# Kernel optimization log

Hardware: AMD Instinct MI355X
Metric: run time of the kernel (lower is better)

The kernel has to match this reference:

```python
import jax, jax.numpy as jnp
import numpy as np

EMBED = 1024
HEADS = 16
HEAD_DIM = EMBED // HEADS
EPS = 1e-8


def setup_inputs() -> dict:
    key = jax.random.key(0)
    ks = jax.random.split(key, 10)
    s = 1.0 / np.sqrt(EMBED)
    return {
        "hidden_input": jax.random.normal(ks[0], (4, 2048, EMBED), dtype=jnp.float32),
        "Wq": jax.random.uniform(ks[1], (EMBED, EMBED), jnp.float32, -s, s),
        "bq": jax.random.uniform(ks[2], (EMBED,), jnp.float32, -s, s),
        "Wk": jax.random.uniform(ks[3], (EMBED, EMBED), jnp.float32, -s, s),
        "bk": jax.random.uniform(ks[4], (EMBED,), jnp.float32, -s, s),
        "Wv": jax.random.uniform(ks[5], (EMBED, EMBED), jnp.float32, -s, s),
        "bv": jax.random.uniform(ks[6], (EMBED,), jnp.float32, -s, s),
        "Wp": jax.random.uniform(ks[7], (EMBED, EMBED), jnp.float32, -s, s),
        "bp": jax.random.uniform(ks[8], (EMBED,), jnp.float32, -s, s),
        "gamma": jnp.ones((EMBED,), jnp.float32),
        "beta": jnp.zeros((EMBED,), jnp.float32),
    }


def reference(hidden_input, Wq, bq, Wk, bk, Wv, bv, Wp, bp, gamma, beta):
    n, l, e = hidden_input.shape
    h, d = HEADS, HEAD_DIM

    def split_heads(x):  # [n, l, e] -> [n, h, l, d]
        return x.reshape(n, l, h, d).transpose(0, 2, 1, 3)

    q = split_heads(hidden_input @ Wq + bq)
    k = split_heads(hidden_input @ Wk + bk)
    v = split_heads(hidden_input @ Wv + bv)

    scores = jnp.einsum("nhqd,nhkd->nhqk", q, k) / jnp.sqrt(jnp.float32(d))
    attn = jax.nn.softmax(scores, axis=-1)
    ctx = jnp.einsum("nhqk,nhkd->nhqd", attn, v)
    ctx = ctx.transpose(0, 2, 1, 3).reshape(n, l, e)

    out = ctx @ Wp + bp
    x = out + hidden_input
    mu = jnp.mean(x, axis=-1, keepdims=True)
    var = jnp.mean(jnp.square(x - mu), axis=-1, keepdims=True)
    return (x - mu) / jnp.sqrt(var + EPS) * gamma + beta
```

## Files before the change

### kernel.cpp

```cpp
#include <hip/hip_runtime.h>

#define EMBED 1024
#define SEQ   2048
#define BATCH 4
#define HEADS 16

typedef __attribute__((ext_vector_type(8))) short short8;
typedef __attribute__((ext_vector_type(4))) float floatx4;
typedef __attribute__((ext_vector_type(16))) float floatx16;

#define MFMA16(a, b, c) __builtin_amdgcn_mfma_f32_16x16x32_bf16((a), (b), (c), 0, 0, 0)
#define MFMA32(a, b, c) __builtin_amdgcn_mfma_f32_32x32x16_bf16((a), (b), (c), 0, 0, 0)
#define ATT_SCALE (0.125f * 1.44269504088896340736f)

static __device__ __forceinline__ unsigned short f2bf(float f) {
  union { float f; unsigned int u; } v; v.f = f;
  unsigned int u = v.u;
  u += 0x7fffu + ((u >> 16) & 1u);
  return (unsigned short)(u >> 16);
}

static __device__ __forceinline__ unsigned cvtpk(float lo, float hi) {
  unsigned r;
  asm("v_cvt_pk_bf16_f32 %0, %1, %2" : "=v"(r) : "v"(lo), "v"(hi));
  return r;
}

static __device__ __forceinline__ void async16(const unsigned short* g, unsigned short* l) {
  __builtin_amdgcn_global_load_lds(
      (const __attribute__((address_space(1))) void*)g,
      (__attribute__((address_space(3))) void*)l, 16, 0, 0);
}

__global__ __launch_bounds__(256) void k_prep(const float* __restrict__ hid,
                                              unsigned short* __restrict__ hidA,
                                              const float* __restrict__ Wq, const float* __restrict__ Wk,
                                              const float* __restrict__ Wv, const float* __restrict__ Wp,
                                              unsigned short* __restrict__ WT) {
  __shared__ unsigned short tile[64][65];
  const int bid = blockIdx.x, tid = threadIdx.x;
  if (bid < 4096) {
    int i = bid * 256 + tid;
    const float4* s = (const float4*)hid;
    float4 a = s[i * 2], b = s[i * 2 + 1];
    uint4 o;
    o.x = (unsigned)f2bf(a.x) | ((unsigned)f2bf(a.y) << 16);
    o.y = (unsigned)f2bf(a.z) | ((unsigned)f2bf(a.w) << 16);
    o.z = (unsigned)f2bf(b.x) | ((unsigned)f2bf(b.y) << 16);
    o.w = (unsigned)f2bf(b.z) | ((unsigned)f2bf(b.w) << 16);
    ((uint4*)hidA)[i] = o;
    return;
  }
  const int idx = bid - 4096;
  const int z = idx >> 8, rem = idx & 255;
  const float* src = (z == 0) ? Wq : (z == 1) ? Wk : (z == 2) ? Wv : Wp;
  unsigned short* dst = WT + (size_t)z * EMBED * EMBED;
  const int k0 = (rem & 15) * 64, n0 = (rem >> 4) * 64;
  for (int i = tid; i < 4096; i += 256) {
    int r = i >> 6, c = i & 63;
    tile[c][r] = f2bf(src[(size_t)(k0 + r) * EMBED + n0 + c]);
  }
  __syncthreads();
  for (int i = tid; i < 4096; i += 256) {
    int r = i >> 6, c = i & 63;
    dst[(size_t)(n0 + r) * EMBED + k0 + c] = tile[r][c];
  }
}

__global__ __launch_bounds__(256) void k_gemm_qkv(const unsigned short* __restrict__ A,
                                                  const unsigned short* __restrict__ BT,
                                                  const float* __restrict__ bq,
                                                  const float* __restrict__ bk,
                                                  const float* __restrict__ bv,
                                                  unsigned short* __restrict__ C) {
  __shared__ unsigned short Als[128 * 64];
  __shared__ unsigned short Bls[128 * 64];
  const int tid = threadIdx.x;
  const int m0 = blockIdx.x * 128, n0 = blockIdx.y * 128;
  const int w = tid >> 6, lane = tid & 63, l16 = lane & 15, quad = lane >> 4;
  const int l7 = l16 & 7;
  const int wrow = (w >> 1) * 64, wcol = (w & 1) * 64;

  floatx4 acc[4][4];
#pragma unroll
  for (int i = 0; i < 4; ++i)
#pragma unroll
    for (int j = 0; j < 4; ++j) acc[i][j] = {0.f, 0.f, 0.f, 0.f};

  const int srow = tid >> 3;
  const int scol = (((tid & 7) ^ (srow & 7)) * 8);
  const unsigned short* Ap = A + (size_t)(m0 + srow) * EMBED + scol;
  const unsigned short* Bp = BT + (size_t)(n0 + srow) * EMBED + scol;

  int ab[2], bb[2];
#pragma unroll
  for (int kc = 0; kc < 2; ++kc) {
    ab[kc] = (wrow + l16) * 64 + (((4 * kc + quad) ^ l7) << 3);
    bb[kc] = (wcol + l16) * 64 + (((4 * kc + quad) ^ l7) << 3);
  }

  for (int kt = 0; kt < 16; ++kt) {
    const int k0 = kt * 64;
#pragma unroll
    for (int i = 0; i < 4; ++i)
      async16(Ap + k0 + (size_t)i * 32 * EMBED, Als + i * 2048 + tid * 8);
#pragma unroll
    for (int i = 0; i < 4; ++i)
      async16(Bp + k0 + (size_t)i * 32 * EMBED, Bls + i * 2048 + tid * 8);
    __syncthreads();
    short8 af[4][2], bf[4][2];
#pragma unroll
    for (int mt = 0; mt < 4; ++mt)
#pragma unroll
      for (int kc = 0; kc < 2; ++kc)
        af[mt][kc] = *(const short8*)(Als + ab[kc] + mt * 1024);
#pragma unroll
    for (int nt = 0; nt < 4; ++nt)
#pragma unroll
      for (int kc = 0; kc < 2; ++kc)
        bf[nt][kc] = *(const short8*)(Bls + bb[kc] + nt * 1024);
#pragma unroll
    for (int kc = 0; kc < 2; ++kc)
#pragma unroll
      for (int mt = 0; mt < 4; ++mt)
#pragma unroll
        for (int nt = 0; nt < 4; ++nt)
          acc[mt][nt] = MFMA16(af[mt][kc], bf[nt][kc], acc[mt][nt]);
    __syncthreads();
  }

  const float* bsel = (n0 < 1024) ? bq : (n0 < 2048 ? bk : bv);
  const float scl = (n0 < 1024) ? ATT_SCALE : 1.0f;
  const int nb = n0 & 1023;
  float bias[4];
#pragma unroll
  for (int nt = 0; nt < 4; ++nt) bias[nt] = bsel[nb + wcol + nt * 16 + l16];
#pragma unroll
  for (int mt = 0; mt < 4; ++mt)
#pragma unroll
    for (int r = 0; r < 4; ++r) {
      int gm = m0 + wrow + mt * 16 + quad * 4 + r;
      size_t base = (size_t)gm * 3072 + n0 + wcol;
#pragma unroll
      for (int nt = 0; nt < 4; ++nt)
        C[base + nt * 16 + l16] = f2bf((acc[mt][nt][r] + bias[nt]) * scl);
    }
}

__global__ __launch_bounds__(256) void k_vt(const unsigned short* __restrict__ QKV,
                                            unsigned short* __restrict__ VT) {
  int lt = blockIdx.x;
  int bh = blockIdx.y;
  int b = bh >> 4, h = bh & 15;
  int l0 = lt * 64;
  __shared__ unsigned short tile[64][65];
  const unsigned short* src = QKV + (size_t)(b * SEQ) * 3072 + 2048 + h * 64;
  unsigned short* dst = VT + (size_t)bh * 64 * SEQ;
  int tid = threadIdx.x;
  for (int i = tid; i < 4096; i += 256) {
    int r = i >> 6, c = i & 63;
    tile[c][r] = src[(size_t)(l0 + r) * 3072 + c];
  }
  __syncthreads();
  for (int i = tid; i < 4096; i += 256) {
    int r = i >> 6, c = i & 63;
    dst[(size_t)r * SEQ + l0 + c] = tile[r][c];
  }
}

__global__ __launch_bounds__(256, 2) void k_attn(const unsigned short* __restrict__ QKV,
                                                 const unsigned short* __restrict__ VT,
                                                 unsigned short* __restrict__ CTX) {
  const int bh = blockIdx.x, qt = blockIdx.y;
  const int b = bh >> 4, h = bh & 15;
  const int tid = threadIdx.x;
  const int w = tid >> 6, lane = tid & 63;
  const int l32 = lane & 31, hi = lane >> 5;

  __shared__ unsigned short Kls[2][64 * 64];
  __shared__ unsigned short Vls[2][64 * 64];
  __shared__ float rsls[4][64];

  const unsigned short* Qb = QKV + (size_t)(b * SEQ + qt * 256 + w * 64) * 3072 + h * 64;
  const unsigned short* Kb = QKV + (size_t)(b * SEQ) * 3072 + 1024 + h * 64;
  const unsigned short* Vb = VT + (size_t)bh * 64 * SEQ;

  short8 qf[2][4];
#pragma unroll
  for (int qg = 0; qg < 2; ++qg)
#pragma unroll
    for (int ds = 0; ds < 4; ++ds)
      qf[qg][ds] = *(const short8*)(Qb + (size_t)(qg * 32 + l32) * 3072 + ds * 16 + hi * 8);

  floatx16 o[2][2];
  float rs[2] = {0.f, 0.f};
#pragma unroll
  for (int qg = 0; qg < 2; ++qg)
#pragma unroll
    for (int dg = 0; dg < 2; ++dg)
#pragma unroll
      for (int c = 0; c < 16; ++c) o[qg][dg][c] = 0.f;

  const int srow = tid >> 3;
  const int scol = (((tid & 7) ^ (srow & 7)) * 8);

  async16(Kb + (size_t)srow * 3072 + scol, Kls[0] + tid * 8);
  async16(Kb + (size_t)(32 + srow) * 3072 + scol, Kls[0] + 2048 + tid * 8);
  async16(Vb + (size_t)srow * SEQ + scol, Vls[0] + tid * 8);
  async16(Vb + (size_t)(32 + srow) * SEQ + scol, Vls[0] + 2048 + tid * 8);
  __syncthreads();

  int cur = 0;
  for (int kt = 0; kt < 32; ++kt) {
    if (kt < 31) {
      const int kn = (kt + 1) * 64;
      unsigned short* Kd = Kls[cur ^ 1];
      unsigned short* Vd = Vls[cur ^ 1];
      async16(Kb + (size_t)(kn + srow) * 3072 + scol, Kd + tid * 8);
      async16(Kb + (size_t)(kn + 32 + srow) * 3072 + scol, Kd + 2048 + tid * 8);
      async16(Vb + (size_t)srow * SEQ + kn + scol, Vd + tid * 8);
      async16(Vb + (size_t)(32 + srow) * SEQ + kn + scol, Vd + 2048 + tid * 8);
    }
    const unsigned short* Kc = Kls[cur];
    const unsigned short* Vc = Vls[cur];

    short8 pa[2][4];
#pragma unroll
    for (int kvg = 0; kvg < 2; ++kvg) {
      short8 kf[4];
#pragma unroll
      for (int ds = 0; ds < 4; ++ds) {
        const int row = kvg * 32 + l32;
        kf[ds] = *(const short8*)(Kc + row * 64 + (((ds * 2 + hi) ^ (row & 7)) << 3));
      }
#pragma unroll
      for (int qg = 0; qg < 2; ++qg) {
        floatx16 s;
#pragma unroll
        for (int c = 0; c < 16; ++c) s[c] = 0.f;
#pragma unroll
        for (int ds = 0; ds < 4; ++ds) s = MFMA32(kf[ds], qf[qg][ds], s);
        float p[16];
#pragma unroll
        for (int c = 0; c < 16; ++c) p[c] = __builtin_amdgcn_exp2f(s[c]);
        rs[qg] += (((p[0] + p[1]) + (p[2] + p[3])) + ((p[4] + p[5]) + (p[6] + p[7])))
                + (((p[8] + p[9]) + (p[10] + p[11])) + ((p[12] + p[13]) + (p[14] + p[15])));
#pragma unroll
        for (int half = 0; half < 2; ++half) {
          unsigned w0 = cvtpk(p[half * 8 + 0], p[half * 8 + 1]);
          unsigned w1 = cvtpk(p[half * 8 + 2], p[half * 8 + 3]);
          unsigned w2 = cvtpk(p[half * 8 + 4], p[half * 8 + 5]);
          unsigned w3 = cvtpk(p[half * 8 + 6], p[half * 8 + 7]);
          asm("v_permlane32_swap_b32 %0, %1" : "+v"(w0), "+v"(w2));
          asm("v_permlane32_swap_b32 %0, %1" : "+v"(w1), "+v"(w3));
          union { unsigned u[4]; short8 s8; } pk;
          pk.u[0] = w0; pk.u[1] = w1; pk.u[2] = w2; pk.u[3] = w3;
          pa[qg][kvg * 2 + half] = pk.s8;
        }
      }
    }

#pragma unroll
    for (int dg = 0; dg < 2; ++dg) {
      short8 vf[4];
#pragma unroll
      for (int ks = 0; ks < 4; ++ks) {
        const int row = dg * 32 + l32;
        vf[ks] = *(const short8*)(Vc + row * 64 + (((ks * 2 + hi) ^ (row & 7)) << 3));
      }
#pragma unroll
      for (int qg = 0; qg < 2; ++qg)
#pragma unroll
        for (int ks = 0; ks < 4; ++ks)
          o[qg][dg] = MFMA32(pa[qg][ks], vf[ks], o[qg][dg]);
    }

    __syncthreads();
    cur ^= 1;
  }

  rs[0] += __shfl_xor(rs[0], 32);
  rs[1] += __shfl_xor(rs[1], 32);
  if (lane < 32) {
    rsls[w][l32] = rs[0];
    rsls[w][32 + l32] = rs[1];
  }

#pragma unroll
  for (int qg = 0; qg < 2; ++qg)
#pragma unroll
    for (int j = 0; j < 16; ++j) {
      const int rl = (j & 3) + 8 * (j >> 2) + 4 * hi;
      const float inv = 1.f / rsls[w][qg * 32 + rl];
      const int gq = b * SEQ + qt * 256 + w * 64 + qg * 32 + rl;
      const size_t base = (size_t)gq * EMBED + h * 64;
#pragma unroll
      for (int dg = 0; dg < 2; ++dg)
        CTX[base + dg * 32 + l32] = f2bf(o[qg][dg][j] * inv);
    }
}

__global__ __launch_bounds__(256) void k_gemm_proj(const unsigned short* __restrict__ A,
                                                   const unsigned short* __restrict__ BT,
                                                   const float* __restrict__ bp,
                                                   const float* __restrict__ hid,
                                                   float* __restrict__ X) {
  __shared__ unsigned short Als[128 * 64];
  __shared__ unsigned short Bls[128 * 64];
  const int tid = threadIdx.x;
  const int m0 = blockIdx.x * 128, n0 = blockIdx.y * 128;
  const int w = tid >> 6, lane = tid & 63, l16 = lane & 15, quad = lane >> 4;
  const int l7 = l16 & 7;
  const int wrow = (w >> 1) * 64, wcol = (w & 1) * 64;

  floatx4 acc[4][4];
#pragma unroll
  for (int i = 0; i < 4; ++i)
#pragma unroll
    for (int j = 0; j < 4; ++j) acc[i][j] = {0.f, 0.f, 0.f, 0.f};

  const int srow = tid >> 3;
  const int scol = (((tid & 7) ^ (srow & 7)) * 8);
  const unsigned short* Ap = A + (size_t)(m0 + srow) * EMBED + scol;
  const unsigned short* Bp = BT + (size_t)(n0 + srow) * EMBED + scol;

  int ab[2], bb[2];
#pragma unroll
  for (int kc = 0; kc < 2; ++kc) {
    ab[kc] = (wrow + l16) * 64 + (((4 * kc + quad) ^ l7) << 3);
    bb[kc] = (wcol + l16) * 64 + (((4 * kc + quad) ^ l7) << 3);
  }

  for (int kt = 0; kt < 16; ++kt) {
    const int k0 = kt * 64;
#pragma unroll
    for (int i = 0; i < 4; ++i)
      async16(Ap + k0 + (size_t)i * 32 * EMBED, Als + i * 2048 + tid * 8);
#pragma unroll
    for (int i = 0; i < 4; ++i)
      async16(Bp + k0 + (size_t)i * 32 * EMBED, Bls + i * 2048 + tid * 8);
    __syncthreads();
    short8 af[4][2], bf[4][2];
#pragma unroll
    for (int mt = 0; mt < 4; ++mt)
#pragma unroll
      for (int kc = 0; kc < 2; ++kc)
        af[mt][kc] = *(const short8*)(Als + ab[kc] + mt * 1024);
#pragma unroll
    for (int nt = 0; nt < 4; ++nt)
#pragma unroll
      for (int kc = 0; kc < 2; ++kc)
        bf[nt][kc] = *(const short8*)(Bls + bb[kc] + nt * 1024);
#pragma unroll
    for (int kc = 0; kc < 2; ++kc)
#pragma unroll
      for (int mt = 0; mt < 4; ++mt)
#pragma unroll
        for (int nt = 0; nt < 4; ++nt)
          acc[mt][nt] = MFMA16(af[mt][kc], bf[nt][kc], acc[mt][nt]);
    __syncthreads();
  }

  float bias[4];
#pragma unroll
  for (int nt = 0; nt < 4; ++nt) bias[nt] = bp[n0 + wcol + nt * 16 + l16];
#pragma unroll
  for (int mt = 0; mt < 4; ++mt)
#pragma unroll
    for (int r = 0; r < 4; ++r) {
      int gm = m0 + wrow + mt * 16 + quad * 4 + r;
      size_t base = (size_t)gm * EMBED + n0 + wcol;
#pragma unroll
      for (int nt = 0; nt < 4; ++nt) {
        size_t idx = base + nt * 16 + l16;
        X[idx] = acc[mt][nt][r] + bias[nt] + hid[idx];
      }
    }
}

__global__ __launch_bounds__(256) void k_ln(float* __restrict__ x,
                                            const float* __restrict__ gamma,
                                            const float* __restrict__ beta) {
  int row = blockIdx.x, tid = threadIdx.x;
  float4* rp = (float4*)(x + (size_t)row * EMBED);
  float4 v = rp[tid];
  float s = v.x + v.y + v.z + v.w;
  float q = v.x * v.x + v.y * v.y + v.z * v.z + v.w * v.w;
#pragma unroll
  for (int off = 1; off < 64; off <<= 1) {
    s += __shfl_xor(s, off);
    q += __shfl_xor(q, off);
  }
  __shared__ float ss[4], sq[4];
  int w = tid >> 6;
  if ((tid & 63) == 0) { ss[w] = s; sq[w] = q; }
  __syncthreads();
  s = ss[0] + ss[1] + ss[2] + ss[3];
  q = sq[0] + sq[1] + sq[2] + sq[3];
  float mean = s * (1.f / 1024.f);
  float var = q * (1.f / 1024.f) - mean * mean;
  float rstd = rsqrtf(var + 1e-8f);
  float4 g = ((const float4*)gamma)[tid];
  float4 be = ((const float4*)beta)[tid];
  v.x = (v.x - mean) * rstd * g.x + be.x;
  v.y = (v.y - mean) * rstd * g.y + be.y;
  v.z = (v.z - mean) * rstd * g.z + be.z;
  v.w = (v.w - mean) * rstd * g.w + be.w;
  rp[tid] = v;
}

extern "C" void kernel_launch(void* const* d_in, const int* in_sizes, int n_in,
                              void* d_out, int out_size, void* d_ws, size_t ws_size,
                              hipStream_t stream) {
  const float* hid   = (const float*)d_in[0];
  const float* Wq    = (const float*)d_in[1];
  const float* bq    = (const float*)d_in[2];
  const float* Wk    = (const float*)d_in[3];
  const float* bk    = (const float*)d_in[4];
  const float* Wv    = (const float*)d_in[5];
  const float* bv    = (const float*)d_in[6];
  const float* Wp    = (const float*)d_in[7];
  const float* bp    = (const float*)d_in[8];
  const float* gamma = (const float*)d_in[9];
  const float* beta  = (const float*)d_in[10];
  float* out = (float*)d_out;

  char* ws = (char*)d_ws;
  unsigned short* hidA = (unsigned short*)ws;
  unsigned short* WT   = (unsigned short*)(ws + (size_t)(16 << 20));
  unsigned short* QKV  = (unsigned short*)(ws + (size_t)(24 << 20));
  unsigned short* VT   = (unsigned short*)(ws + (size_t)(72 << 20));
  unsigned short* CTX  = (unsigned short*)(ws + (size_t)(88 << 20));

  k_prep<<<5120, 256, 0, stream>>>(hid, hidA, Wq, Wk, Wv, Wp, WT);
  k_gemm_qkv<<<dim3(64, 24), 256, 0, stream>>>(hidA, WT, bq, bk, bv, QKV);
  k_vt<<<dim3(32, 64), 256, 0, stream>>>(QKV, VT);
  k_attn<<<dim3(64, 8), 256, 0, stream>>>(QKV, VT, CTX);
  k_gemm_proj<<<dim3(64, 8), 256, 0, stream>>>(CTX, WT + (size_t)3 * EMBED * EMBED, bp, hid, out);
  k_ln<<<8192, 256, 0, stream>>>(out, gamma, beta);
}
```

Before: 279.3 us.

## Split attention KV range across two blocks and add a combine kernel

The attention kernel now splits the 2048-key range into two halves along a new grid z dimension. Each half writes an unnormalized bf16 partial context and its per-row exp sums to workspace. A new k_comb kernel adds the two partials, normalizes them and writes CTX. Launch bounds rise to 4 blocks per CU to double parallelism and occupancy. The cost is extra global traffic and a launch for the partials, a bf16 rounding step on unnormalized partials, and possible register pressure or spills from the tighter launch bound.

```diff
diff --git a/kernel.cpp b/kernel.cpp
--- a/kernel.cpp
+++ b/kernel.cpp
@@ -18,6 +18,13 @@
   unsigned int u = v.u;
   u += 0x7fffu + ((u >> 16) & 1u);
   return (unsigned short)(u >> 16);
+}
+
+static __device__ __forceinline__ float bf2f_lo(unsigned u) {
+  union { unsigned u; float f; } v; v.u = u << 16; return v.f;
+}
+static __device__ __forceinline__ float bf2f_hi(unsigned u) {
+  union { unsigned u; float f; } v; v.u = u & 0xffff0000u; return v.f;
 }
 
 static __device__ __forceinline__ unsigned cvtpk(float lo, float hi) {
@@ -168,10 +175,12 @@
   }
 }
 
-__global__ __launch_bounds__(256, 2) void k_attn(const unsigned short* __restrict__ QKV,
+__global__ __launch_bounds__(256, 4) void k_attn(const unsigned short* __restrict__ QKV,
                                                  const unsigned short* __restrict__ VT,
-                                                 unsigned short* __restrict__ CTX) {
-  const int bh = blockIdx.x, qt = blockIdx.y;
+                                                 unsigned short* __restrict__ OP0,
+                                                 unsigned short* __restrict__ OP1,
+                                                 float* __restrict__ RSP) {
+  const int bh = blockIdx.x, qt = blockIdx.y, hv = blockIdx.z;
   const int b = bh >> 4, h = bh & 15;
   const int tid = threadIdx.x;
   const int w = tid >> 6, lane = tid & 63;
@@ -179,7 +188,6 @@
 
   __shared__ unsigned short Kls[2][64 * 64];
   __shared__ unsigned short Vls[2][64 * 64];
-  __shared__ float rsls[4][64];
 
   const unsigned short* Qb = QKV + (size_t)(b * SEQ + qt * 256 + w * 64) * 3072 + h * 64;
   const unsigned short* Kb = QKV + (size_t)(b * SEQ) * 3072 + 1024 + h * 64;
@@ -203,17 +211,21 @@
 
   const int srow = tid >> 3;
   const int scol = (((tid & 7) ^ (srow & 7)) * 8);
-
-  async16(Kb + (size_t)srow * 3072 + scol, Kls[0] + tid * 8);
-  async16(Kb + (size_t)(32 + srow) * 3072 + scol, Kls[0] + 2048 + tid * 8);
-  async16(Vb + (size_t)srow * SEQ + scol, Vls[0] + tid * 8);
-  async16(Vb + (size_t)(32 + srow) * SEQ + scol, Vls[0] + 2048 + tid * 8);
+  const int kbase = hv * 16;
+
+  {
+    const int kv0 = kbase * 64;
+    async16(Kb + (size_t)(kv0 + srow) * 3072 + scol, Kls[0] + tid * 8);
+    async16(Kb + (size_t)(kv0 + 32 + srow) * 3072 + scol, Kls[0] + 2048 + tid * 8);
+    async16(Vb + (size_t)srow * SEQ + kv0 + scol, Vls[0] + tid * 8);
+    async16(Vb + (size_t)(32 + srow) * SEQ + kv0 + scol, Vls[0] + 2048 + tid * 8);
+  }
   __syncthreads();
 
   int cur = 0;
-  for (int kt = 0; kt < 32; ++kt) {
-    if (kt < 31) {
-      const int kn = (kt + 1) * 64;
+  for (int kt = 0; kt < 16; ++kt) {
+    if (kt < 15) {
+      const int kn = (kbase + kt + 1) * 64;
       unsigned short* Kd = Kls[cur ^ 1];
       unsigned short* Vd = Vls[cur ^ 1];
       async16(Kb + (size_t)(kn + srow) * 3072 + scol, Kd + tid * 8);
@@ -282,22 +294,45 @@
   rs[0] += __shfl_xor(rs[0], 32);
   rs[1] += __shfl_xor(rs[1], 32);
   if (lane < 32) {
-    rsls[w][l32] = rs[0];
-    rsls[w][32 + l32] = rs[1];
-  }
-
+    float* rp = RSP + ((size_t)(hv * 64 + bh)) * SEQ + qt * 256 + w * 64;
+    rp[l32] = rs[0];
+    rp[32 + l32] = rs[1];
+  }
+
+  unsigned short* Od = hv ? OP1 : OP0;
 #pragma unroll
   for (int qg = 0; qg < 2; ++qg)
 #pragma unroll
     for (int j = 0; j < 16; ++j) {
       const int rl = (j & 3) + 8 * (j >> 2) + 4 * hi;
-      const float inv = 1.f / rsls[w][qg * 32 + rl];
       const int gq = b * SEQ + qt * 256 + w * 64 + qg * 32 + rl;
       const size_t base = (size_t)gq * EMBED + h * 64;
 #pragma unroll
       for (int dg = 0; dg < 2; ++dg)
-        CTX[base + dg * 32 + l32] = f2bf(o[qg][dg][j] * inv);
-    }
+        Od[base + dg * 32 + l32] = f2bf(o[qg][dg][j]);
+    }
+}
+
+__global__ __launch_bounds__(256) void k_comb(const unsigned short* __restrict__ OP0,
+                                              const unsigned short* __restrict__ OP1,
+                                              const float* __restrict__ RSP,
+                                              unsigned short* __restrict__ CTX) {
+  const int gq = blockIdx.x, tid = threadIdx.x;
+  const int b = gq >> 11, q = gq & 2047;
+  const int col = tid * 4, h = col >> 6;
+  const float inv = 1.f / (RSP[((size_t)(b * 16 + h)) * SEQ + q] +
+                           RSP[((size_t)(64 + b * 16 + h)) * SEQ + q]);
+  const size_t base = (size_t)gq * EMBED + col;
+  uint2 ua = *(const uint2*)(OP0 + base);
+  uint2 ub = *(const uint2*)(OP1 + base);
+  float c0 = (bf2f_lo(ua.x) + bf2f_lo(ub.x)) * inv;
+  float c1 = (bf2f_hi(ua.x) + bf2f_hi(ub.x)) * inv;
+  float c2 = (bf2f_lo(ua.y) + bf2f_lo(ub.y)) * inv;
+  float c3 = (bf2f_hi(ua.y) + bf2f_hi(ub.y)) * inv;
+  uint2 oo;
+  oo.x = (unsigned)f2bf(c0) | ((unsigned)f2bf(c1) << 16);
+  oo.y = (unsigned)f2bf(c2) | ((unsigned)f2bf(c3) << 16);
+  *(uint2*)(CTX + base) = oo;
 }
 
 __global__ __launch_bounds__(256) void k_gemm_proj(const unsigned short* __restrict__ A,
@@ -431,11 +466,15 @@
   unsigned short* QKV  = (unsigned short*)(ws + (size_t)(24 << 20));
   unsigned short* VT   = (unsigned short*)(ws + (size_t)(72 << 20));
   unsigned short* CTX  = (unsigned short*)(ws + (size_t)(88 << 20));
+  unsigned short* OP0  = (unsigned short*)ws;
+  unsigned short* OP1  = (unsigned short*)(ws + (size_t)(104 << 20));
+  float*          RSP  = (float*)(ws + (size_t)(120 << 20));
 
   k_prep<<<5120, 256, 0, stream>>>(hid, hidA, Wq, Wk, Wv, Wp, WT);
   k_gemm_qkv<<<dim3(64, 24), 256, 0, stream>>>(hidA, WT, bq, bk, bv, QKV);
   k_vt<<<dim3(32, 64), 256, 0, stream>>>(QKV, VT);
-  k_attn<<<dim3(64, 8), 256, 0, stream>>>(QKV, VT, CTX);
+  k_attn<<<dim3(64, 8, 2), 256, 0, stream>>>(QKV, VT, OP0, OP1, RSP);
+  k_comb<<<8192, 256, 0, stream>>>(OP0, OP1, RSP, CTX);
   k_gemm_proj<<<dim3(64, 8), 256, 0, stream>>>(CTX, WT + (size_t)3 * EMBED * EMBED, bp, hid, out);
   k_ln<<<8192, 256, 0, stream>>>(out, gamma, beta);
 }
```

Measured after the change: 748.6 us. 2.68x slower.

## Halve attention query tile per block to 128 rows, doubling grid and occupancy

Applied to the files above, without the earlier changes.

Each wave in the attention kernel now handles 32 query rows instead of 64, so a block covers 128 queries and the grid doubles to 1024 blocks. Launch bounds rise to 3 blocks per CU because each wave holds fewer accumulators and Q fragments. The aim is more parallelism and occupancy on the 256-CU device, since the previous 512-block grid underfilled it. The cost is that each K/V tile loaded into LDS is reused by half as many queries, which doubles total K/V traffic.

```diff
diff --git a/kernel.cpp b/kernel.cpp
--- a/kernel.cpp
+++ b/kernel.cpp
@@ -168,7 +168,7 @@
   }
 }
 
-__global__ __launch_bounds__(256, 2) void k_attn(const unsigned short* __restrict__ QKV,
+__global__ __launch_bounds__(256, 3) void k_attn(const unsigned short* __restrict__ QKV,
                                                  const unsigned short* __restrict__ VT,
                                                  unsigned short* __restrict__ CTX) {
   const int bh = blockIdx.x, qt = blockIdx.y;
@@ -179,27 +179,23 @@
 
   __shared__ unsigned short Kls[2][64 * 64];
   __shared__ unsigned short Vls[2][64 * 64];
-  __shared__ float rsls[4][64];
-
-  const unsigned short* Qb = QKV + (size_t)(b * SEQ + qt * 256 + w * 64) * 3072 + h * 64;
+  __shared__ float rsls[4][32];
+
+  const unsigned short* Qb = QKV + (size_t)(b * SEQ + qt * 128 + w * 32) * 3072 + h * 64;
   const unsigned short* Kb = QKV + (size_t)(b * SEQ) * 3072 + 1024 + h * 64;
   const unsigned short* Vb = VT + (size_t)bh * 64 * SEQ;
 
-  short8 qf[2][4];
-#pragma unroll
-  for (int qg = 0; qg < 2; ++qg)
-#pragma unroll
-    for (int ds = 0; ds < 4; ++ds)
-      qf[qg][ds] = *(const short8*)(Qb + (size_t)(qg * 32 + l32) * 3072 + ds * 16 + hi * 8);
-
-  floatx16 o[2][2];
-  float rs[2] = {0.f, 0.f};
-#pragma unroll
-  for (int qg = 0; qg < 2; ++qg)
-#pragma unroll
-    for (int dg = 0; dg < 2; ++dg)
-#pragma unroll
-      for (int c = 0; c < 16; ++c) o[qg][dg][c] = 0.f;
+  short8 qf[4];
+#pragma unroll
+  for (int ds = 0; ds < 4; ++ds)
+    qf[ds] = *(const short8*)(Qb + (size_t)l32 * 3072 + ds * 16 + hi * 8);
+
+  floatx16 o[2];
+  float rs = 0.f;
+#pragma unroll
+  for (int dg = 0; dg < 2; ++dg)
+#pragma unroll
+    for (int c = 0; c < 16; ++c) o[dg][c] = 0.f;
 
   const int srow = tid >> 3;
   const int scol = (((tid & 7) ^ (srow & 7)) * 8);
@@ -224,7 +220,7 @@
     const unsigned short* Kc = Kls[cur];
     const unsigned short* Vc = Vls[cur];
 
-    short8 pa[2][4];
+    short8 pa[4];
 #pragma unroll
     for (int kvg = 0; kvg < 2; ++kvg) {
       short8 kf[4];
@@ -233,30 +229,27 @@
         const int row = kvg * 32 + l32;
         kf[ds] = *(const short8*)(Kc + row * 64 + (((ds * 2 + hi) ^ (row & 7)) << 3));
       }
-#pragma unroll
-      for (int qg = 0; qg < 2; ++qg) {
-        floatx16 s;
-#pragma unroll
-        for (int c = 0; c < 16; ++c) s[c] = 0.f;
-#pragma unroll
-        for (int ds = 0; ds < 4; ++ds) s = MFMA32(kf[ds], qf[qg][ds], s);
-        float p[16];
-#pragma unroll
-        for (int c = 0; c < 16; ++c) p[c] = __builtin_amdgcn_exp2f(s[c]);
-        rs[qg] += (((p[0] + p[1]) + (p[2] + p[3])) + ((p[4] + p[5]) + (p[6] + p[7])))
-                + (((p[8] + p[9]) + (p[10] + p[11])) + ((p[12] + p[13]) + (p[14] + p[15])));
-#pragma unroll
-        for (int half = 0; half < 2; ++half) {
-          unsigned w0 = cvtpk(p[half * 8 + 0], p[half * 8 + 1]);
-          unsigned w1 = cvtpk(p[half * 8 + 2], p[half * 8 + 3]);
-          unsigned w2 = cvtpk(p[half * 8 + 4], p[half * 8 + 5]);
-          unsigned w3 = cvtpk(p[half * 8 + 6], p[half * 8 + 7]);
-          asm("v_permlane32_swap_b32 %0, %1" : "+v"(w0), "+v"(w2));
-          asm("v_permlane32_swap_b32 %0, %1" : "+v"(w1), "+v"(w3));
-          union { unsigned u[4]; short8 s8; } pk;
-          pk.u[0] = w0; pk.u[1] = w1; pk.u[2] = w2; pk.u[3] = w3;
-          pa[qg][kvg * 2 + half] = pk.s8;
-        }
+      floatx16 s;
+#pragma unroll
+      for (int c = 0; c < 16; ++c) s[c] = 0.f;
+#pragma unroll
+      for (int ds = 0; ds < 4; ++ds) s = MFMA32(kf[ds], qf[ds], s);
+      float p[16];
+#pragma unroll
+      for (int c = 0; c < 16; ++c) p[c] = __builtin_amdgcn_exp2f(s[c]);
+      rs += (((p[0] + p[1]) + (p[2] + p[3])) + ((p[4] + p[5]) + (p[6] + p[7])))
+          + (((p[8] + p[9]) + (p[10] + p[11])) + ((p[12] + p[13]) + (p[14] + p[15])));
+#pragma unroll
+      for (int half = 0; half < 2; ++half) {
+        unsigned w0 = cvtpk(p[half * 8 + 0], p[half * 8 + 1]);
+        unsigned w1 = cvtpk(p[half * 8 + 2], p[half * 8 + 3]);
+        unsigned w2 = cvtpk(p[half * 8 + 4], p[half * 8 + 5]);
+        unsigned w3 = cvtpk(p[half * 8 + 6], p[half * 8 + 7]);
+        asm("v_permlane32_swap_b32 %0, %1" : "+v"(w0), "+v"(w2));
+        asm("v_permlane32_swap_b32 %0, %1" : "+v"(w1), "+v"(w3));
+        union { unsigned u[4]; short8 s8; } pk;
+        pk.u[0] = w0; pk.u[1] = w1; pk.u[2] = w2; pk.u[3] = w3;
+        pa[kvg * 2 + half] = pk.s8;
       }
     }
 
@@ -269,35 +262,27 @@
         vf[ks] = *(const short8*)(Vc + row * 64 + (((ks * 2 + hi) ^ (row & 7)) << 3));
       }
 #pragma unroll
-      for (int qg = 0; qg < 2; ++qg)
-#pragma unroll
-        for (int ks = 0; ks < 4; ++ks)
-          o[qg][dg] = MFMA32(pa[qg][ks], vf[ks], o[qg][dg]);
+      for (int ks = 0; ks < 4; ++ks)
+        o[dg] = MFMA32(pa[ks], vf[ks], o[dg]);
     }
 
     __syncthreads();
     cur ^= 1;
   }
 
-  rs[0] += __shfl_xor(rs[0], 32);
-  rs[1] += __shfl_xor(rs[1], 32);
-  if (lane < 32) {
-    rsls[w][l32] = rs[0];
-    rsls[w][32 + l32] = rs[1];
-  }
-
-#pragma unroll
-  for (int qg = 0; qg < 2; ++qg)
-#pragma unroll
-    for (int j = 0; j < 16; ++j) {
-      const int rl = (j & 3) + 8 * (j >> 2) + 4 * hi;
-      const float inv = 1.f / rsls[w][qg * 32 + rl];
-      const int gq = b * SEQ + qt * 256 + w * 64 + qg * 32 + rl;
-      const size_t base = (size_t)gq * EMBED + h * 64;
-#pragma unroll
-      for (int dg = 0; dg < 2; ++dg)
-        CTX[base + dg * 32 + l32] = f2bf(o[qg][dg][j] * inv);
-    }
+  rs += __shfl_xor(rs, 32);
+  if (lane < 32) rsls[w][l32] = rs;
+
+#pragma unroll
+  for (int j = 0; j < 16; ++j) {
+    const int rl = (j & 3) + 8 * (j >> 2) + 4 * hi;
+    const float inv = 1.f / rsls[w][rl];
+    const int gq = b * SEQ + qt * 128 + w * 32 + rl;
+    const size_t base = (size_t)gq * EMBED + h * 64;
+#pragma unroll
+    for (int dg = 0; dg < 2; ++dg)
+      CTX[base + dg * 32 + l32] = f2bf(o[dg][j] * inv);
+  }
 }
 
 __global__ __launch_bounds__(256) void k_gemm_proj(const unsigned short* __restrict__ A,
@@ -435,7 +420,7 @@
   k_prep<<<5120, 256, 0, stream>>>(hid, hidA, Wq, Wk, Wv, Wp, WT);
   k_gemm_qkv<<<dim3(64, 24), 256, 0, stream>>>(hidA, WT, bq, bk, bv, QKV);
   k_vt<<<dim3(32, 64), 256, 0, stream>>>(QKV, VT);
-  k_attn<<<dim3(64, 8), 256, 0, stream>>>(QKV, VT, CTX);
+  k_attn<<<dim3(64, 16), 256, 0, stream>>>(QKV, VT, CTX);
   k_gemm_proj<<<dim3(64, 8), 256, 0, stream>>>(CTX, WT + (size_t)3 * EMBED * EMBED, bp, hid, out);
   k_ln<<<8192, 256, 0, stream>>>(out, gamma, beta);
 }
```

New measurement: 305.7 us. 1.09x slower.

## Rewrite QKV GEMM with 256x256 tiles, double-buffered LDS and phased MFMA

Applied to the files above, without the earlier changes.

The QKV projection GEMM moves from 128x128 tiles with 4 waves to 256x256 tiles with 8 waves. It double-buffers the A and B tiles in LDS so the next k-slice loads asynchronously while the current one is computed. Each k-step is split into four quadrant phases with explicit barriers, waitcnt and raised wave priority around the MFMA bursts. This aims to hide global load latency and raise data reuse per block. It uses 128KB of LDS per block and more accumulator registers, and the grid drops to 384 blocks, which may underfill the GPU.

```diff
diff --git a/kernel.cpp b/kernel.cpp
--- a/kernel.cpp
+++ b/kernel.cpp
@@ -67,66 +67,91 @@
   }
 }
 
-__global__ __launch_bounds__(256) void k_gemm_qkv(const unsigned short* __restrict__ A,
-                                                  const unsigned short* __restrict__ BT,
-                                                  const float* __restrict__ bq,
-                                                  const float* __restrict__ bk,
-                                                  const float* __restrict__ bv,
-                                                  unsigned short* __restrict__ C) {
-  __shared__ unsigned short Als[128 * 64];
-  __shared__ unsigned short Bls[128 * 64];
+__global__ __launch_bounds__(512, 2) void k_gemm_qkv(const unsigned short* __restrict__ A,
+                                                     const unsigned short* __restrict__ BT,
+                                                     const float* __restrict__ bq,
+                                                     const float* __restrict__ bk,
+                                                     const float* __restrict__ bv,
+                                                     unsigned short* __restrict__ C) {
+  __shared__ unsigned short As[2][256 * 64];
+  __shared__ unsigned short Bs[2][256 * 64];
   const int tid = threadIdx.x;
-  const int m0 = blockIdx.x * 128, n0 = blockIdx.y * 128;
+  const int m0 = blockIdx.x * 256, n0 = blockIdx.y * 256;
   const int w = tid >> 6, lane = tid & 63, l16 = lane & 15, quad = lane >> 4;
-  const int l7 = l16 & 7;
-  const int wrow = (w >> 1) * 64, wcol = (w & 1) * 64;
-
-  floatx4 acc[4][4];
-#pragma unroll
-  for (int i = 0; i < 4; ++i)
+  const int wm = w >> 2, wn = w & 3;
+
+  floatx4 acc[8][4];
+#pragma unroll
+  for (int i = 0; i < 8; ++i)
 #pragma unroll
     for (int j = 0; j < 4; ++j) acc[i][j] = {0.f, 0.f, 0.f, 0.f};
 
   const int srow = tid >> 3;
   const int scol = (((tid & 7) ^ (srow & 7)) * 8);
-  const unsigned short* Ap = A + (size_t)(m0 + srow) * EMBED + scol;
-  const unsigned short* Bp = BT + (size_t)(n0 + srow) * EMBED + scol;
-
-  int ab[2], bb[2];
-#pragma unroll
-  for (int kc = 0; kc < 2; ++kc) {
-    ab[kc] = (wrow + l16) * 64 + (((4 * kc + quad) ^ l7) << 3);
-    bb[kc] = (wcol + l16) * 64 + (((4 * kc + quad) ^ l7) << 3);
-  }
-
-  for (int kt = 0; kt < 16; ++kt) {
-    const int k0 = kt * 64;
-#pragma unroll
-    for (int i = 0; i < 4; ++i)
-      async16(Ap + k0 + (size_t)i * 32 * EMBED, Als + i * 2048 + tid * 8);
-#pragma unroll
-    for (int i = 0; i < 4; ++i)
-      async16(Bp + k0 + (size_t)i * 32 * EMBED, Bls + i * 2048 + tid * 8);
-    __syncthreads();
-    short8 af[4][2], bf[4][2];
-#pragma unroll
-    for (int mt = 0; mt < 4; ++mt)
+  const unsigned short* Ag = A + (size_t)(m0 + srow) * EMBED + scol;
+  const unsigned short* Bg = BT + (size_t)(n0 + srow) * EMBED + scol;
+
+  unsigned short* Acur = As[0];
+  unsigned short* Bcur = Bs[0];
+  unsigned short* Anxt = As[1];
+  unsigned short* Bnxt = Bs[1];
+
+#pragma unroll
+  for (int r = 0; r < 4; ++r) async16(Ag + (size_t)r * 64 * EMBED, Acur + r * 4096 + tid * 8);
+#pragma unroll
+  for (int r = 0; r < 4; ++r) async16(Bg + (size_t)r * 64 * EMBED, Bcur + r * 4096 + tid * 8);
+  __asm__ volatile("s_waitcnt vmcnt(0)" ::: "memory");
+  __asm__ volatile("s_barrier" ::: "memory");
+
+  for (int t = 0; t < 16; ++t) {
+    const int last = (t == 15);
+#pragma unroll
+    for (int q = 0; q < 4; ++q) {
+      const int mh = q >> 1, nh = q & 1;
+      if (q == 0 && !last) {
+        const unsigned short* Asrc = Ag + (t + 1) * 64;
+#pragma unroll
+        for (int r = 0; r < 4; ++r) async16(Asrc + (size_t)r * 64 * EMBED, Anxt + r * 4096 + tid * 8);
+      }
+      if (q == 1 && !last) {
+        const unsigned short* Bsrc = Bg + (t + 1) * 64;
+#pragma unroll
+        for (int r = 0; r < 4; ++r) async16(Bsrc + (size_t)r * 64 * EMBED, Bnxt + r * 4096 + tid * 8);
+      }
+      short8 af[4][2], bf[2][2];
+#pragma unroll
+      for (int mi = 0; mi < 4; ++mi)
+#pragma unroll
+        for (int kc = 0; kc < 2; ++kc) {
+          const int row = wm * 128 + (mh * 4 + mi) * 16 + l16;
+          af[mi][kc] = *(const short8*)(Acur + row * 64 + (((kc * 4 + quad) ^ (row & 7)) << 3));
+        }
+#pragma unroll
+      for (int ni = 0; ni < 2; ++ni)
+#pragma unroll
+        for (int kc = 0; kc < 2; ++kc) {
+          const int row = wn * 64 + (nh * 2 + ni) * 16 + l16;
+          bf[ni][kc] = *(const short8*)(Bcur + row * 64 + (((kc * 4 + quad) ^ (row & 7)) << 3));
+        }
+      __asm__ volatile("s_barrier" ::: "memory");
+      __asm__ volatile("s_waitcnt lgkmcnt(0)" ::: "memory");
+      __builtin_amdgcn_sched_barrier(0);
+      __builtin_amdgcn_s_setprio(1);
 #pragma unroll
       for (int kc = 0; kc < 2; ++kc)
-        af[mt][kc] = *(const short8*)(Als + ab[kc] + mt * 1024);
-#pragma unroll
-    for (int nt = 0; nt < 4; ++nt)
-#pragma unroll
-      for (int kc = 0; kc < 2; ++kc)
-        bf[nt][kc] = *(const short8*)(Bls + bb[kc] + nt * 1024);
-#pragma unroll
-    for (int kc = 0; kc < 2; ++kc)
-#pragma unroll
-      for (int mt = 0; mt < 4; ++mt)
-#pragma unroll
-        for (int nt = 0; nt < 4; ++nt)
-          acc[mt][nt] = MFMA16(af[mt][kc], bf[nt][kc], acc[mt][nt]);
-    __syncthreads();
+#pragma unroll
+        for (int mi = 0; mi < 4; ++mi)
+#pragma unroll
+          for (int ni = 0; ni < 2; ++ni)
+            acc[mh * 4 + mi][nh * 2 + ni] =
+                MFMA16(af[mi][kc], bf[ni][kc], acc[mh * 4 + mi][nh * 2 + ni]);
+      __builtin_amdgcn_s_setprio(0);
+      if (q == 3) __asm__ volatile("s_waitcnt vmcnt(0)" ::: "memory");
+      __asm__ volatile("s_barrier" ::: "memory");
+    }
+    unsigned short* tp;
+    tp = Acur; Acur = Anxt; Anxt = tp;
+    tp = Bcur; Bcur = Bnxt; Bnxt = tp;
   }
 
   const float* bsel = (n0 < 1024) ? bq : (n0 < 2048 ? bk : bv);
@@ -134,13 +159,13 @@
   const int nb = n0 & 1023;
   float bias[4];
 #pragma unroll
-  for (int nt = 0; nt < 4; ++nt) bias[nt] = bsel[nb + wcol + nt * 16 + l16];
-#pragma unroll
-  for (int mt = 0; mt < 4; ++mt)
+  for (int nt = 0; nt < 4; ++nt) bias[nt] = bsel[nb + wn * 64 + nt * 16 + l16];
+#pragma unroll
+  for (int mt = 0; mt < 8; ++mt)
 #pragma unroll
     for (int r = 0; r < 4; ++r) {
-      int gm = m0 + wrow + mt * 16 + quad * 4 + r;
-      size_t base = (size_t)gm * 3072 + n0 + wcol;
+      const int gm = m0 + wm * 128 + mt * 16 + quad * 4 + r;
+      const size_t base = (size_t)gm * 3072 + n0 + wn * 64;
 #pragma unroll
       for (int nt = 0; nt < 4; ++nt)
         C[base + nt * 16 + l16] = f2bf((acc[mt][nt][r] + bias[nt]) * scl);
@@ -433,7 +458,7 @@
   unsigned short* CTX  = (unsigned short*)(ws + (size_t)(88 << 20));
 
   k_prep<<<5120, 256, 0, stream>>>(hid, hidA, Wq, Wk, Wv, Wp, WT);
-  k_gemm_qkv<<<dim3(64, 24), 256, 0, stream>>>(hidA, WT, bq, bk, bv, QKV);
+  k_gemm_qkv<<<dim3(32, 12), 512, 0, stream>>>(hidA, WT, bq, bk, bv, QKV);
   k_vt<<<dim3(32, 64), 256, 0, stream>>>(QKV, VT);
   k_attn<<<dim3(64, 8), 256, 0, stream>>>(QKV, VT, CTX);
   k_gemm_proj<<<dim3(64, 8), 256, 0, stream>>>(CTX, WT + (size_t)3 * EMBED * EMBED, bp, hid, out);
```

New measurement: 303.6 us. 1.09x slower.
